# Kernel tuning notes

Hardware: AMD Instinct MI355X
Metric: run time of the kernel (lower is better)

## Reference

```python
import jax, jax.numpy as jnp
import numpy as np

B, S, H = 2, 2048, 2048
NH = 16
NOPE, ROPE, VDIM, RANK = 128, 64, 128, 512
QHD = NOPE + ROPE  # 192
MAX_POS, THETA = 4096, 50000.0
EPS = 1e-6


def rms_norm(x, w):
    var = jnp.mean(x.astype(jnp.float32) ** 2, axis=-1, keepdims=True)
    return (x * jax.lax.rsqrt(var + EPS)).astype(x.dtype) * w


def deinterleave(x):
    # view(..., d//2, 2).transpose(-1,-2).reshape(..., d): [x0,x2,...,x1,x3,...]
    return jnp.concatenate([x[..., ::2], x[..., 1::2]], axis=-1)


def rotate_half(x):
    x1, x2 = jnp.split(x, 2, axis=-1)
    return jnp.concatenate([-x2, x1], axis=-1)


def setup_inputs() -> dict:
    key = jax.random.key(0)
    ks = jax.random.split(key, 6)
    hidden_states = jax.random.normal(ks[0], (B, S, H), dtype=jnp.float32)
    attention_mask = jnp.broadcast_to(jnp.tril(jnp.ones((S, S), dtype=bool))[None, None], (B, 1, S, S))
    position_ids = jnp.broadcast_to(jnp.arange(S, dtype=jnp.int32)[None], (B, S))
    inv_freq = 1.0 / (THETA ** (jnp.arange(0, ROPE, 2, dtype=jnp.float32) / ROPE))
    freqs = jnp.arange(MAX_POS, dtype=jnp.float32)[:, None] * inv_freq[None, :]
    emb = jnp.concatenate([freqs, freqs], axis=-1)
    cos_cache, sin_cache = jnp.cos(emb), jnp.sin(emb)
    Wq = jax.random.normal(ks[1], (H, NH * QHD), dtype=jnp.float32) * 0.02
    Wkv_a = jax.random.normal(ks[2], (H, RANK + ROPE), dtype=jnp.float32) * 0.02
    kv_a_ln_w = jnp.ones((RANK,), dtype=jnp.float32)
    Wkv_b = jax.random.normal(ks[3], (NH, NOPE + VDIM, RANK), dtype=jnp.float32) * 0.02
    Wo = jax.random.normal(ks[4], (NH * VDIM, H), dtype=jnp.float32) * 0.02
    return {"hidden_states": hidden_states, "attention_mask": attention_mask, "position_ids": position_ids,
            "cos_cache": cos_cache, "sin_cache": sin_cache, "Wq": Wq, "Wkv_a": Wkv_a,
            "kv_a_ln_w": kv_a_ln_w, "Wkv_b": Wkv_b, "Wo": Wo}


def reference(hidden_states, attention_mask, position_ids, cos_cache, sin_cache, Wq, Wkv_a, kv_a_ln_w, Wkv_b, Wo):
    bsz, q_len, _ = hidden_states.shape
    scale = QHD ** (-0.5)
    # Q projection: [b,s,h*192] -> [b,h,s,192]
    q = (hidden_states @ Wq).reshape(bsz, q_len, NH, QHD).transpose(0, 2, 1, 3)
    q_nope, q_pe = q[..., :NOPE], q[..., NOPE:]
    # compressed KV + shared rope key: [b,s,576]
    ckv_full = hidden_states @ Wkv_a
    compressed_kv, k_pe = ckv_full[..., :RANK], ckv_full[..., RANK:]
    compressed_kv = rms_norm(compressed_kv, kv_a_ln_w)  # [b,s,512]
    # interleaved -> half layout, then standard RoPE
    q_pe = deinterleave(q_pe)                     # [b,h,s,64]
    k_pe = deinterleave(k_pe)                     # [b,s,64]
    cos = cos_cache[position_ids][:, None]        # [b,1,s,64]
    sin = sin_cache[position_ids][:, None]
    q_pe = q_pe * cos + rotate_half(q_pe) * sin
    k_pe = (k_pe[:, None] * cos + rotate_half(k_pe[:, None]) * sin)[:, 0]  # [b,s,64]
    # weight absorption
    q_absorb = Wkv_b[:, :NOPE]    # [h,128,512]
    out_absorb = Wkv_b[:, NOPE:]  # [h,128,512]
    q_nope_c = jnp.einsum('hdc,bhqd->bhqc', q_absorb, q_nope)  # [b,h,s,512]
    scores = (jnp.einsum('bhqd,bkd->bhqk', q_pe, k_pe)
              + jnp.einsum('bhqc,bkc->bhqk', q_nope_c, compressed_kv)) * scale
    scores = jnp.where(attention_mask, scores, jnp.float32(-1e9))
    probs = jax.nn.softmax(scores.astype(jnp.float32), axis=-1).astype(hidden_states.dtype)
    x = jnp.einsum('bhqk,bkc->bhqc', probs, compressed_kv)     # [b,h,s,512]
    attn = jnp.einsum('bhqc,hdc->bhqd', x, out_absorb)         # [b,h,s,128]
    attn = attn.transpose(0, 2, 1, 3).reshape(bsz, q_len, NH * VDIM)
    return attn @ Wo
```

## Files before the change

kernel.cpp:

```cpp
#include <hip/hip_runtime.h>
#include <math.h>

#define B_    2
#define S_    2048
#define H_    2048
#define NH_   16
#define NOPE_ 128
#define ROPE_ 64
#define VDIM_ 128
#define RANK_ 512
#define QHD_  192
#define DTOT_ 576

typedef short short8 __attribute__((ext_vector_type(8)));
typedef float f32x4 __attribute__((ext_vector_type(4)));

__device__ __forceinline__ unsigned short f2bf(float f) {
    unsigned u = __float_as_uint(f);
    u += 0x7fffu + ((u >> 16) & 1u);
    return (unsigned short)(u >> 16);
}
__device__ __forceinline__ float bf2f(unsigned short u) {
    return __uint_as_float((unsigned)u << 16);
}
__device__ __forceinline__ unsigned pack2bf(float a, float b) {
    return (unsigned)f2bf(a) | ((unsigned)f2bf(b) << 16);
}
__device__ __forceinline__ unsigned long long pack4bf(float a, float b, float c, float d) {
    return (unsigned long long)pack2bf(a, b) | ((unsigned long long)pack2bf(c, d) << 32);
}
union i4s8 { int4 i; short8 s; };

typedef __attribute__((address_space(3))) unsigned int lds_u32_t;
typedef __attribute__((address_space(1))) const unsigned int glob_u32_t;
__device__ __forceinline__ void async_copy16(const unsigned short* g, unsigned short* l) {
    __builtin_amdgcn_global_load_lds((glob_u32_t*)g, (lds_u32_t*)l, 16, 0, 0);
}

__global__ __launch_bounds__(256) void cast_bf16(const float* __restrict__ in,
                                                 unsigned short* __restrict__ out)
{
    const size_t i = ((size_t)blockIdx.x * 256 + threadIdx.x) * 4;
    float4 v = *(const float4*)(in + i);
    *(unsigned long long*)(out + i) = pack4bf(v.x, v.y, v.z, v.w);
}

__global__ __launch_bounds__(256) void transpose_w(const float* __restrict__ in,
                                                   unsigned short* __restrict__ out,
                                                   int Rr, int Cc,
                                                   size_t inBatch, size_t outBatch)
{
    __shared__ unsigned short tl[64][72];
    in  += (size_t)blockIdx.z * inBatch;
    out += (size_t)blockIdx.z * outBatch;
    const int t  = threadIdx.x;
    const int r0 = blockIdx.x * 64;
    const int c0 = blockIdx.y * 64;
    const int lr = t >> 4;
    const int lc = (t & 15) * 4;
#pragma unroll
    for (int r = 0; r < 4; ++r) {
        float4 v = *(const float4*)(in + (size_t)(r0 + lr*4 + r) * Cc + c0 + lc);
        tl[lr*4 + r][lc+0] = f2bf(v.x); tl[lr*4 + r][lc+1] = f2bf(v.y);
        tl[lr*4 + r][lc+2] = f2bf(v.z); tl[lr*4 + r][lc+3] = f2bf(v.w);
    }
    __syncthreads();
#pragma unroll
    for (int r = 0; r < 4; ++r) {
        ushort4 v;
        v.x = tl[lc+0][lr*4+r]; v.y = tl[lc+1][lr*4+r];
        v.z = tl[lc+2][lr*4+r]; v.w = tl[lc+3][lr*4+r];
        *(ushort4*)(out + (size_t)(c0 + lr*4 + r) * Rr + r0 + lc) = v;
    }
}

#define BGEMM_BODY(STORE_STMT)                                                     \
    __shared__ unsigned short Al[128*32];                                          \
    __shared__ unsigned short Bl[128*32];                                          \
    const int t = threadIdx.x;                                                     \
    const int wv = t >> 6;                                                         \
    const int lane = t & 63;                                                       \
    const int lq = lane & 15, quad = lane >> 4;                                    \
    const int m0 = blockIdx.y * 128, n0 = blockIdx.x * 128;                        \
    const int wrow = (wv >> 1) * 64, wcol = (wv & 1) * 64;                         \
    const int srow = lane >> 2;                                                    \
    const int scol = (lane & 3) * 8;                                               \
    f32x4 acc[4][4] = {};                                                          \
    for (int k0 = 0; k0 < K; k0 += 32) {                                           \
        _Pragma("unroll")                                                          \
        for (int pA = 0; pA < 2; ++pA) {                                           \
            const unsigned short* src =                                            \
                A + (size_t)(m0 + pA*64 + wv*16 + srow) * lda + k0 + scol;         \
            async_copy16(src, &Al[pA*2048 + wv*512]);                              \
        }                                                                          \
        _Pragma("unroll")                                                          \
        for (int pB = 0; pB < 2; ++pB) {                                           \
            int brow = n0 + pB*64 + wv*16 + srow;                                  \
            if (brow > N - 1) brow = N - 1;                                        \
            const unsigned short* src = B + (size_t)brow * ldb + k0 + scol;        \
            async_copy16(src, &Bl[pB*2048 + wv*512]);                              \
        }                                                                          \
        __syncthreads();                                                           \
        short8 af[4], bf[4];                                                       \
        _Pragma("unroll")                                                          \
        for (int i = 0; i < 4; ++i) {                                              \
            af[i] = *(const short8*)&Al[(wrow + i*16 + lq)*32 + quad*8];           \
            bf[i] = *(const short8*)&Bl[(wcol + i*16 + lq)*32 + quad*8];           \
        }                                                                          \
        _Pragma("unroll")                                                          \
        for (int mi = 0; mi < 4; ++mi)                                             \
            _Pragma("unroll")                                                      \
            for (int ni = 0; ni < 4; ++ni)                                         \
                acc[mi][ni] = __builtin_amdgcn_mfma_f32_16x16x32_bf16(             \
                    af[mi], bf[ni], acc[mi][ni], 0, 0, 0);                         \
        __syncthreads();                                                           \
    }                                                                              \
    _Pragma("unroll")                                                              \
    for (int mi = 0; mi < 4; ++mi)                                                 \
        _Pragma("unroll")                                                          \
        for (int ni = 0; ni < 4; ++ni) {                                           \
            int col = n0 + wcol + ni*16 + lq;                                      \
            if (col < N) {                                                         \
                _Pragma("unroll")                                                  \
                for (int r = 0; r < 4; ++r)                                        \
                    STORE_STMT;                                                    \
            }                                                                      \
        }

__global__ __launch_bounds__(256, 2) void bgemm2(const unsigned short* __restrict__ A,
                                                 int lda,
                                                 const unsigned short* __restrict__ B,
                                                 int ldb,
                                                 unsigned short* __restrict__ C,
                                                 int ldc, int K, int N, int qcmode)
{
    if (qcmode == 1) {
        const int z = blockIdx.z;
        A += (size_t)(z >> 4) * S_ * (NH_*QHD_) + (z & 15) * QHD_;
        B += (size_t)(z & 15) * RANK_ * NOPE_;
        C += (size_t)z * S_ * DTOT_;
    } else if (qcmode == 2) {
        const int z = blockIdx.z;
        A += (size_t)(z & 15) * 256 * RANK_ + (size_t)NOPE_ * RANK_;
        B += (size_t)(z >> 4) * S_ * DTOT_;
        C += (size_t)z * VDIM_ * S_;
    }
    BGEMM_BODY(C[(size_t)(m0 + wrow + mi*16 + quad*4 + r) * ldc + col] = f2bf(acc[mi][ni][r]))
}

__global__ __launch_bounds__(256, 2) void bgemm2f(const unsigned short* __restrict__ A,
                                                  int lda,
                                                  const unsigned short* __restrict__ B,
                                                  int ldb,
                                                  float* __restrict__ C,
                                                  int ldc, int K, int N)
{
    BGEMM_BODY(C[(size_t)(m0 + wrow + mi*16 + quad*4 + r) * ldc + col] = acc[mi][ni][r])
}

__global__ __launch_bounds__(128) void postkv(const unsigned short* __restrict__ ckv_bf,
                                              const float* __restrict__ lnw,
                                              const int*   __restrict__ pos_ids,
                                              const float* __restrict__ cosc,
                                              const float* __restrict__ sinc,
                                              unsigned short* __restrict__ k_cat)
{
    const int row = blockIdx.x;
    const int t   = threadIdx.x;
    const unsigned short* src = ckv_bf + (size_t)row * DTOT_;
    __shared__ float red[128];

    ushort4 v = *(const ushort4*)(src + t * 4);
    float x0 = bf2f(v.x), x1 = bf2f(v.y), x2 = bf2f(v.z), x3 = bf2f(v.w);
    red[t] = x0*x0 + x1*x1 + x2*x2 + x3*x3;
    __syncthreads();
    for (int off = 64; off > 0; off >>= 1) {
        if (t < off) red[t] += red[t + off];
        __syncthreads();
    }
    const float rs = rsqrtf(red[0] / (float)RANK_ + 1e-6f);

    unsigned short* kc = k_cat + (size_t)row * DTOT_;
    *(unsigned long long*)(kc + t*4) =
        pack4bf(x0*rs*lnw[t*4+0], x1*rs*lnw[t*4+1], x2*rs*lnw[t*4+2], x3*rs*lnw[t*4+3]);

    if (t < 32) {
        const int pos = pos_ids[row];
        const float c  = cosc[pos * ROPE_ + t];
        const float sn = sinc[pos * ROPE_ + t];
        const float y0 = bf2f(src[RANK_ + 2*t]);
        const float y1 = bf2f(src[RANK_ + 2*t + 1]);
        kc[RANK_ + t]      = f2bf(y0*c - y1*sn);
        kc[RANK_ + 32 + t] = f2bf(y1*c + y0*sn);
    }
}

__global__ __launch_bounds__(512) void ropeq(const unsigned short* __restrict__ q_bf,
                                             const int*   __restrict__ pos_ids,
                                             const float* __restrict__ cosc,
                                             const float* __restrict__ sinc,
                                             unsigned short* __restrict__ q_cat)
{
    const int row = blockIdx.x;
    const int t   = threadIdx.x;
    const int h   = t >> 5;
    const int i   = t & 31;
    const int pos = pos_ids[row];
    const float c  = cosc[pos * ROPE_ + i];
    const float sn = sinc[pos * ROPE_ + i];
    const unsigned short* qrow = q_bf + (size_t)row * (NH_*QHD_) + h * QHD_ + NOPE_;
    const float x0 = bf2f(qrow[2*i]);
    const float x1 = bf2f(qrow[2*i + 1]);
    const int b = row >> 11, s = row & 2047;
    unsigned short* qc = q_cat + ((size_t)(b * NH_ + h) * S_ + s) * DTOT_ + RANK_;
    qc[i]      = f2bf(x0*c - x1*sn);
    qc[32 + i] = f2bf(x1*c + x0*sn);
}

__global__ __launch_bounds__(256) void wcast(const float* __restrict__ w,
                                             unsigned short* __restrict__ wbf)
{
    const size_t i = ((size_t)blockIdx.x * 256 + threadIdx.x) * 4;
    float4 v = *(const float4*)(w + i);
    *(unsigned long long*)(wbf + i) = pack4bf(v.x, v.y, v.z, v.w);
}

__device__ __forceinline__ short8 quad_transpose(unsigned d0, unsigned d1,
                                                 unsigned d2, unsigned d3,
                                                 int srcA, int srcB, bool lowquad)
{
    int e0 = __shfl((int)d0, srcA, 64);
    int e1 = __shfl((int)d1, srcA, 64);
    int e2 = __shfl((int)d2, srcA, 64);
    int e3 = __shfl((int)d3, srcA, 64);
    int f0 = __shfl((int)d0, srcB, 64);
    int f1 = __shfl((int)d1, srcB, 64);
    int f2 = __shfl((int)d2, srcB, 64);
    int f3 = __shfl((int)d3, srcB, 64);
    i4s8 u;
    u.i.x = lowquad ? e0 : e2;
    u.i.y = lowquad ? e1 : e3;
    u.i.z = lowquad ? f0 : f2;
    u.i.w = lowquad ? f1 : f3;
    return u.s;
}

__global__ __launch_bounds__(256, 2) void flash_attn4(
    const unsigned short* __restrict__ q_cat,
    const unsigned short* __restrict__ k_cat,
    const unsigned short* __restrict__ vwt,
    unsigned short* __restrict__ attn_bf)
{
    __shared__ unsigned short sKa[32*512];
    __shared__ unsigned short sKb[32*64];
    __shared__ unsigned short sVW[128*32];

    const int t    = threadIdx.x;
    const int wv   = t >> 6;
    const int lane = t & 63;
    const int lq   = lane & 15;
    const int quad = lane >> 4;
    const int h    = blockIdx.x;
    const int q0   = (31 - blockIdx.y) * 64;
    const int b    = blockIdx.z;
    const int srcA = lq + ((quad & 1) << 5);
    const int srcB = srcA + 16;
    const bool lowq = quad < 2;
    const int myq  = q0 + wv*16 + lq;

    const unsigned short* qrow =
        q_cat + (((size_t)(b*NH_ + h)) * S_ + q0 + wv*16 + lq) * DTOT_ + quad*8;
    short8 qf[18];
#pragma unroll
    for (int c = 0; c < 18; ++c) qf[c] = *(const short8*)(qrow + c*32);

    const unsigned short* kcb = k_cat + (size_t)b * S_ * DTOT_;
    const unsigned short* vtb = vwt + (size_t)(b*NH_ + h) * VDIM_ * S_;

    f32x4 o[8];
#pragma unroll
    for (int i = 0; i < 8; ++i) o[i] = (f32x4){0.f, 0.f, 0.f, 0.f};
    float m_i = -1e30f, l_i = 0.f;
    const float scale = 0.0721687836f;
    const int ntiles = (q0 >> 5) + 2;

    const int swz  = lq & 7;
    const int selA = (swz >> 2) * 32;
    const int selB = 32 - selA;
    const int kqo  = (quad ^ (swz & 3)) * 8;
    const unsigned short* kr0a = &sKa[lq*512 + kqo];
    const unsigned short* kr1a = &sKa[(16 + lq)*512 + kqo];
    const unsigned short* kr0b = &sKb[lq*64 + kqo];
    const unsigned short* kr1b = &sKb[(16 + lq)*64 + kqo];

    const int kq0 = wv*DTOT_ + (lane ^ wv)*8;
    const int kq1 = wv*DTOT_ + (lane ^ (wv + 4))*8;
    const int kob = (t >> 3)*DTOT_ + RANK_ + ((t & 7) ^ ((t >> 3) & 7))*8;

    const int vrow  = wv*16 + (lane >> 2);
    const int vgcol = (((lane & 3) ^ ((lane >> 3) & 3))) * 8;
    const int pvsw  = (quad ^ ((lq >> 1) & 3)) * 8;

#define ISSUE_K(TPTR)                                                          \
    _Pragma("unroll")                                                          \
    for (int p = 0; p < 8; ++p)                                                \
        async_copy16((TPTR) + (p*4)*DTOT_ + ((p & 1) ? kq1 : kq0),             \
                     &sKa[p*2048 + wv*512]);                                   \
    async_copy16((TPTR) + kob, &sKb[wv*512])

    const unsigned short* ktp = kcb;
    ISSUE_K(ktp);
    ktp += 32 * DTOT_;

    for (int tt = 0; tt < ntiles; ++tt) {
        const int k0 = tt << 5;
        __syncthreads();
        {
#pragma unroll
            for (int p = 0; p < 2; ++p) {
                const unsigned short* vsrc =
                    vtb + (size_t)(p*64 + vrow) * S_ + k0 + vgcol;
                async_copy16(vsrc, &sVW[p*2048 + wv*512]);
            }
        }
        f32x4 s0a = {0.f,0.f,0.f,0.f}, s0b = {0.f,0.f,0.f,0.f};
        f32x4 s1a = {0.f,0.f,0.f,0.f}, s1b = {0.f,0.f,0.f,0.f};
#pragma unroll
        for (int c = 0; c < 16; c += 2) {
            short8 ka0 = *(const short8*)(kr0a + c*32 + selA);
            short8 kb0 = *(const short8*)(kr0a + c*32 + selB);
            short8 ka1 = *(const short8*)(kr1a + c*32 + selA);
            short8 kb1 = *(const short8*)(kr1a + c*32 + selB);
            s0a = __builtin_amdgcn_mfma_f32_16x16x32_bf16(ka0, qf[c],   s0a, 0, 0, 0);
            s1a = __builtin_amdgcn_mfma_f32_16x16x32_bf16(ka1, qf[c],   s1a, 0, 0, 0);
            s0b = __builtin_amdgcn_mfma_f32_16x16x32_bf16(kb0, qf[c+1], s0b, 0, 0, 0);
            s1b = __builtin_amdgcn_mfma_f32_16x16x32_bf16(kb1, qf[c+1], s1b, 0, 0, 0);
        }
        {
            short8 ka0 = *(const short8*)(kr0b + selA);
            short8 kb0 = *(const short8*)(kr0b + selB);
            short8 ka1 = *(const short8*)(kr1b + selA);
            short8 kb1 = *(const short8*)(kr1b + selB);
            s0a = __builtin_amdgcn_mfma_f32_16x16x32_bf16(ka0, qf[16], s0a, 0, 0, 0);
            s1a = __builtin_amdgcn_mfma_f32_16x16x32_bf16(ka1, qf[16], s1a, 0, 0, 0);
            s0b = __builtin_amdgcn_mfma_f32_16x16x32_bf16(kb0, qf[17], s0b, 0, 0, 0);
            s1b = __builtin_amdgcn_mfma_f32_16x16x32_bf16(kb1, qf[17], s1b, 0, 0, 0);
        }
        float sv[8];
#pragma unroll
        for (int r = 0; r < 4; ++r) {
            int kk0 = k0 + quad*4 + r;
            sv[r]     = (kk0      <= myq) ? (s0a[r] + s0b[r]) * scale : -1e30f;
            sv[r + 4] = (kk0 + 16 <= myq) ? (s1a[r] + s1b[r]) * scale : -1e30f;
        }
        float mx = sv[0];
#pragma unroll
        for (int i = 1; i < 8; ++i) mx = fmaxf(mx, sv[i]);
        mx = fmaxf(mx, __shfl_xor(mx, 16));
        mx = fmaxf(mx, __shfl_xor(mx, 32));
        if (!__all(mx <= m_i + 8.f)) {
            const float m_new = fmaxf(m_i, mx);
            const float alpha = __expf(m_i - m_new);
            m_i = m_new;
            l_i *= alpha;
#pragma unroll
            for (int i = 0; i < 8; ++i) {
                o[i][0]*=alpha; o[i][1]*=alpha; o[i][2]*=alpha; o[i][3]*=alpha;
            }
        }
        float p[8]; float ls = 0.f;
#pragma unroll
        for (int i = 0; i < 8; ++i) { p[i] = __expf(sv[i] - m_i); ls += p[i]; }
        ls += __shfl_xor(ls, 16);
        ls += __shfl_xor(ls, 32);
        l_i += ls;
        short8 pb = quad_transpose(pack2bf(p[0], p[1]), pack2bf(p[2], p[3]),
                                   pack2bf(p[4], p[5]), pack2bf(p[6], p[7]),
                                   srcA, srcB, lowq);
        __syncthreads();
        if (tt + 1 < ntiles) {
            ISSUE_K(ktp);
            ktp += 32 * DTOT_;
        }
#pragma unroll
        for (int dt = 0; dt < 8; ++dt) {
            short8 va = *(const short8*)&sVW[(dt*16 + lq)*32 + pvsw];
            o[dt] = __builtin_amdgcn_mfma_f32_16x16x32_bf16(va, pb, o[dt], 0, 0, 0);
        }
    }

    const float inv = 1.0f / l_i;
    unsigned short* orow =
        attn_bf + ((size_t)b * S_ + q0 + wv*16 + lq) * (NH_*VDIM_) + h*VDIM_;
#pragma unroll
    for (int dt2 = 0; dt2 < 4; ++dt2) {
        short8 xa = quad_transpose(
            pack2bf(o[2*dt2][0]*inv,   o[2*dt2][1]*inv),
            pack2bf(o[2*dt2][2]*inv,   o[2*dt2][3]*inv),
            pack2bf(o[2*dt2+1][0]*inv, o[2*dt2+1][1]*inv),
            pack2bf(o[2*dt2+1][2]*inv, o[2*dt2+1][3]*inv),
            srcA, srcB, lowq);
        *(short8*)(orow + dt2*32 + quad*8) = xa;
    }
}

extern "C" void kernel_launch(void* const* d_in, const int* in_sizes, int n_in,
                              void* d_out, int out_size, void* d_ws, size_t ws_size,
                              hipStream_t stream)
{
    const float* hidden  = (const float*)d_in[0];
    const int*   pos_ids = (const int*)d_in[2];
    const float* cosc    = (const float*)d_in[3];
    const float* sinc    = (const float*)d_in[4];
    const float* Wq      = (const float*)d_in[5];
    const float* Wkv_a   = (const float*)d_in[6];
    const float* lnw     = (const float*)d_in[7];
    const float* Wkv_b   = (const float*)d_in[8];
    const float* Wo      = (const float*)d_in[9];
    float* out = (float*)d_out;

    const int M = B_ * S_;
    char* ws = (char*)d_ws;
    unsigned short* hidden_bf = (unsigned short*)ws;
    unsigned short* vwT       = (unsigned short*)ws;
    unsigned short* q_bf      = (unsigned short*)(ws + 16777216);
    unsigned short* attn_bf   = q_bf;
    unsigned short* ckv_bf    = (unsigned short*)(ws + 41943040);
    unsigned short* wqaT      = ckv_bf;
    unsigned short* q_cat     = (unsigned short*)(ws + 46661632);
    unsigned short* k_cat     = (unsigned short*)(ws + 122159104);
    unsigned short* wT        = (unsigned short*)(ws + 126877696);
    unsigned short* w2bf      = (unsigned short*)(ws + 126877696 + 8388608);

    cast_bf16<<<8192, 256, 0, stream>>>(hidden, hidden_bf);
    transpose_w<<<dim3(32, 48, 1), 256, 0, stream>>>(Wq, wT, H_, NH_*QHD_, 0, 0);
    bgemm2<<<dim3(24, 32, 1), 256, 0, stream>>>(hidden_bf, H_, wT, H_, q_bf, NH_*QHD_, H_, NH_*QHD_, 0);
    transpose_w<<<dim3(32, 9, 1), 256, 0, stream>>>(Wkv_a, wT, H_, DTOT_, 0, 0);
    bgemm2<<<dim3(5, 32, 1), 256, 0, stream>>>(hidden_bf, H_, wT, H_, ckv_bf, DTOT_, H_, DTOT_, 0);
    postkv<<<M, 128, 0, stream>>>(ckv_bf, lnw, pos_ids, cosc, sinc, k_cat);
    ropeq<<<M, 512, 0, stream>>>(q_bf, pos_ids, cosc, sinc, q_cat);
    wcast<<<(NH_*256*RANK_)/1024, 256, 0, stream>>>(Wkv_b, w2bf);
    bgemm2<<<dim3(16, 1, 32), 256, 0, stream>>>(w2bf, RANK_, k_cat, DTOT_, vwT, S_, RANK_, S_, 2);
    transpose_w<<<dim3(2, 8, 16), 256, 0, stream>>>(Wkv_b, wqaT, NOPE_, RANK_,
                                                    (size_t)256*RANK_, (size_t)RANK_*NOPE_);
    bgemm2<<<dim3(4, 16, 32), 256, 0, stream>>>(q_bf, NH_*QHD_, wqaT, NOPE_, q_cat, DTOT_, NOPE_, RANK_, 1);
    flash_attn4<<<dim3(NH_, S_/64, B_), 256, 0, stream>>>(q_cat, k_cat, vwT, attn_bf);
    transpose_w<<<dim3(32, 32, 1), 256, 0, stream>>>(Wo, wT, H_, H_, 0, 0);
    bgemm2f<<<dim3(16, 32, 1), 256, 0, stream>>>(attn_bf, H_, wT, H_, out, H_, H_, H_);
}
```

Before: 523.6 us.

## Process two 64-row query strips per attention block to reuse K/V tiles

The flash attention kernel now handles 128 query rows per block: each wave keeps a second 16-row query group whose Q fragments are read from global memory inside the loop, along with a second set of online-softmax state and output accumulators. Each K/V tile staged in LDS is reused by twice as many queries, which halves the grid and the total K/V load traffic. The strip order is also reversed for one batch so heavy and light causal strips interleave across the grid. The costs are much higher register pressure from the doubled accumulators, repeated global loads of the second Q group on every tile, fewer blocks to balance the causal work, and a few extra masked tiles at the diagonal.

Result: slower. 621.2 us (+18.7%).

```diff
diff --git a/kernel.cpp b/kernel.cpp
--- a/kernel.cpp
+++ b/kernel.cpp
@@ -122,7 +122,7 @@
             int col = n0 + wcol + ni*16 + lq;                                      \
             if (col < N) {                                                         \
                 _Pragma("unroll")                                                  \
-                for (int r = 0; r < 4; ++r)                                        \
+                for (int r = 0; r < 4; ++r)                                       \
                     STORE_STMT;                                                    \
             }                                                                      \
         }
@@ -261,28 +261,33 @@
     const int lq   = lane & 15;
     const int quad = lane >> 4;
     const int h    = blockIdx.x;
-    const int q0   = (31 - blockIdx.y) * 64;
     const int b    = blockIdx.z;
+    const int ystrip = b ? blockIdx.y : (15 - blockIdx.y);
+    const int q0   = ystrip * 128;
     const int srcA = lq + ((quad & 1) << 5);
     const int srcB = srcA + 16;
     const bool lowq = quad < 2;
-    const int myq  = q0 + wv*16 + lq;
+    const int myq0 = q0 + wv*16 + lq;
 
     const unsigned short* qrow =
         q_cat + (((size_t)(b*NH_ + h)) * S_ + q0 + wv*16 + lq) * DTOT_ + quad*8;
     short8 qf[18];
 #pragma unroll
     for (int c = 0; c < 18; ++c) qf[c] = *(const short8*)(qrow + c*32);
+    const unsigned short* q1row = qrow + (size_t)64 * DTOT_;
 
     const unsigned short* kcb = k_cat + (size_t)b * S_ * DTOT_;
     const unsigned short* vtb = vwt + (size_t)(b*NH_ + h) * VDIM_ * S_;
 
-    f32x4 o[8];
-#pragma unroll
-    for (int i = 0; i < 8; ++i) o[i] = (f32x4){0.f, 0.f, 0.f, 0.f};
-    float m_i = -1e30f, l_i = 0.f;
+    f32x4 o0[8], o1[8];
+#pragma unroll
+    for (int i = 0; i < 8; ++i) {
+        o0[i] = (f32x4){0.f, 0.f, 0.f, 0.f};
+        o1[i] = (f32x4){0.f, 0.f, 0.f, 0.f};
+    }
+    float mi0 = -1e30f, li0 = 0.f, mi1 = -1e30f, li1 = 0.f;
     const float scale = 0.0721687836f;
-    const int ntiles = (q0 >> 5) + 2;
+    const int ntiles = (q0 >> 5) + 4;
 
     const int swz  = lq & 7;
     const int selA = (swz >> 2) * 32;
@@ -325,58 +330,89 @@
         }
         f32x4 s0a = {0.f,0.f,0.f,0.f}, s0b = {0.f,0.f,0.f,0.f};
         f32x4 s1a = {0.f,0.f,0.f,0.f}, s1b = {0.f,0.f,0.f,0.f};
+        f32x4 u0a = {0.f,0.f,0.f,0.f}, u0b = {0.f,0.f,0.f,0.f};
+        f32x4 u1a = {0.f,0.f,0.f,0.f}, u1b = {0.f,0.f,0.f,0.f};
 #pragma unroll
         for (int c = 0; c < 16; c += 2) {
             short8 ka0 = *(const short8*)(kr0a + c*32 + selA);
             short8 kb0 = *(const short8*)(kr0a + c*32 + selB);
             short8 ka1 = *(const short8*)(kr1a + c*32 + selA);
             short8 kb1 = *(const short8*)(kr1a + c*32 + selB);
+            short8 g1a = *(const short8*)(q1row + c*32);
+            short8 g1b = *(const short8*)(q1row + (c+1)*32);
             s0a = __builtin_amdgcn_mfma_f32_16x16x32_bf16(ka0, qf[c],   s0a, 0, 0, 0);
             s1a = __builtin_amdgcn_mfma_f32_16x16x32_bf16(ka1, qf[c],   s1a, 0, 0, 0);
             s0b = __builtin_amdgcn_mfma_f32_16x16x32_bf16(kb0, qf[c+1], s0b, 0, 0, 0);
             s1b = __builtin_amdgcn_mfma_f32_16x16x32_bf16(kb1, qf[c+1], s1b, 0, 0, 0);
+            u0a = __builtin_amdgcn_mfma_f32_16x16x32_bf16(ka0, g1a,     u0a, 0, 0, 0);
+            u1a = __builtin_amdgcn_mfma_f32_16x16x32_bf16(ka1, g1a,     u1a, 0, 0, 0);
+            u0b = __builtin_amdgcn_mfma_f32_16x16x32_bf16(kb0, g1b,     u0b, 0, 0, 0);
+            u1b = __builtin_amdgcn_mfma_f32_16x16x32_bf16(kb1, g1b,     u1b, 0, 0, 0);
         }
         {
             short8 ka0 = *(const short8*)(kr0b + selA);
             short8 kb0 = *(const short8*)(kr0b + selB);
             short8 ka1 = *(const short8*)(kr1b + selA);
             short8 kb1 = *(const short8*)(kr1b + selB);
+            short8 g1a = *(const short8*)(q1row + 16*32);
+            short8 g1b = *(const short8*)(q1row + 17*32);
             s0a = __builtin_amdgcn_mfma_f32_16x16x32_bf16(ka0, qf[16], s0a, 0, 0, 0);
             s1a = __builtin_amdgcn_mfma_f32_16x16x32_bf16(ka1, qf[16], s1a, 0, 0, 0);
             s0b = __builtin_amdgcn_mfma_f32_16x16x32_bf16(kb0, qf[17], s0b, 0, 0, 0);
             s1b = __builtin_amdgcn_mfma_f32_16x16x32_bf16(kb1, qf[17], s1b, 0, 0, 0);
-        }
-        float sv[8];
+            u0a = __builtin_amdgcn_mfma_f32_16x16x32_bf16(ka0, g1a,    u0a, 0, 0, 0);
+            u1a = __builtin_amdgcn_mfma_f32_16x16x32_bf16(ka1, g1a,    u1a, 0, 0, 0);
+            u0b = __builtin_amdgcn_mfma_f32_16x16x32_bf16(kb0, g1b,    u0b, 0, 0, 0);
+            u1b = __builtin_amdgcn_mfma_f32_16x16x32_bf16(kb1, g1b,    u1b, 0, 0, 0);
+        }
+        float sv0[8], sv1[8];
 #pragma unroll
         for (int r = 0; r < 4; ++r) {
             int kk0 = k0 + quad*4 + r;
-            sv[r]     = (kk0      <= myq) ? (s0a[r] + s0b[r]) * scale : -1e30f;
-            sv[r + 4] = (kk0 + 16 <= myq) ? (s1a[r] + s1b[r]) * scale : -1e30f;
-        }
-        float mx = sv[0];
-#pragma unroll
-        for (int i = 1; i < 8; ++i) mx = fmaxf(mx, sv[i]);
-        mx = fmaxf(mx, __shfl_xor(mx, 16));
-        mx = fmaxf(mx, __shfl_xor(mx, 32));
-        if (!__all(mx <= m_i + 8.f)) {
-            const float m_new = fmaxf(m_i, mx);
-            const float alpha = __expf(m_i - m_new);
-            m_i = m_new;
-            l_i *= alpha;
+            sv0[r]     = (kk0      <= myq0)      ? (s0a[r] + s0b[r]) * scale : -1e30f;
+            sv0[r + 4] = (kk0 + 16 <= myq0)      ? (s1a[r] + s1b[r]) * scale : -1e30f;
+            sv1[r]     = (kk0      <= myq0 + 64) ? (u0a[r] + u0b[r]) * scale : -1e30f;
+            sv1[r + 4] = (kk0 + 16 <= myq0 + 64) ? (u1a[r] + u1b[r]) * scale : -1e30f;
+        }
+        float mx0 = sv0[0], mx1 = sv1[0];
+#pragma unroll
+        for (int i = 1; i < 8; ++i) { mx0 = fmaxf(mx0, sv0[i]); mx1 = fmaxf(mx1, sv1[i]); }
+        mx0 = fmaxf(mx0, __shfl_xor(mx0, 16));
+        mx0 = fmaxf(mx0, __shfl_xor(mx0, 32));
+        mx1 = fmaxf(mx1, __shfl_xor(mx1, 16));
+        mx1 = fmaxf(mx1, __shfl_xor(mx1, 32));
+        if (!__all(mx0 <= mi0 + 8.f)) {
+            const float m_new = fmaxf(mi0, mx0);
+            const float alpha = __expf(mi0 - m_new);
+            mi0 = m_new; li0 *= alpha;
 #pragma unroll
             for (int i = 0; i < 8; ++i) {
-                o[i][0]*=alpha; o[i][1]*=alpha; o[i][2]*=alpha; o[i][3]*=alpha;
+                o0[i][0]*=alpha; o0[i][1]*=alpha; o0[i][2]*=alpha; o0[i][3]*=alpha;
             }
         }
-        float p[8]; float ls = 0.f;
-#pragma unroll
-        for (int i = 0; i < 8; ++i) { p[i] = __expf(sv[i] - m_i); ls += p[i]; }
-        ls += __shfl_xor(ls, 16);
-        ls += __shfl_xor(ls, 32);
-        l_i += ls;
-        short8 pb = quad_transpose(pack2bf(p[0], p[1]), pack2bf(p[2], p[3]),
-                                   pack2bf(p[4], p[5]), pack2bf(p[6], p[7]),
-                                   srcA, srcB, lowq);
+        if (!__all(mx1 <= mi1 + 8.f)) {
+            const float m_new = fmaxf(mi1, mx1);
+            const float alpha = __expf(mi1 - m_new);
+            mi1 = m_new; li1 *= alpha;
+#pragma unroll
+            for (int i = 0; i < 8; ++i) {
+                o1[i][0]*=alpha; o1[i][1]*=alpha; o1[i][2]*=alpha; o1[i][3]*=alpha;
+            }
+        }
+        float p0[8], p1[8]; float ls0 = 0.f, ls1 = 0.f;
+#pragma unroll
+        for (int i = 0; i < 8; ++i) {
+            p0[i] = __expf(sv0[i] - mi0); ls0 += p0[i];
+            p1[i] = __expf(sv1[i] - mi1); ls1 += p1[i];
+        }
+        ls0 += __shfl_xor(ls0, 16); ls0 += __shfl_xor(ls0, 32); li0 += ls0;
+        ls1 += __shfl_xor(ls1, 16); ls1 += __shfl_xor(ls1, 32); li1 += ls1;
+        short8 pb0 = quad_transpose(pack2bf(p0[0], p0[1]), pack2bf(p0[2], p0[3]),
+                                    pack2bf(p0[4], p0[5]), pack2bf(p0[6], p0[7]),
+                                    srcA, srcB, lowq);
+        short8 pb1 = quad_transpose(pack2bf(p1[0], p1[1]), pack2bf(p1[2], p1[3]),
+                                    pack2bf(p1[4], p1[5]), pack2bf(p1[6], p1[7]),
+                                    srcA, srcB, lowq);
         __syncthreads();
         if (tt + 1 < ntiles) {
             ISSUE_K(ktp);
@@ -385,22 +421,32 @@
 #pragma unroll
         for (int dt = 0; dt < 8; ++dt) {
             short8 va = *(const short8*)&sVW[(dt*16 + lq)*32 + pvsw];
-            o[dt] = __builtin_amdgcn_mfma_f32_16x16x32_bf16(va, pb, o[dt], 0, 0, 0);
-        }
-    }
-
-    const float inv = 1.0f / l_i;
+            o0[dt] = __builtin_amdgcn_mfma_f32_16x16x32_bf16(va, pb0, o0[dt], 0, 0, 0);
+            o1[dt] = __builtin_amdgcn_mfma_f32_16x16x32_bf16(va, pb1, o1[dt], 0, 0, 0);
+        }
+    }
+
+    const float inv0 = 1.0f / li0;
+    const float inv1 = 1.0f / li1;
     unsigned short* orow =
         attn_bf + ((size_t)b * S_ + q0 + wv*16 + lq) * (NH_*VDIM_) + h*VDIM_;
+    unsigned short* orow1 = orow + (size_t)64 * (NH_*VDIM_);
 #pragma unroll
     for (int dt2 = 0; dt2 < 4; ++dt2) {
         short8 xa = quad_transpose(
-            pack2bf(o[2*dt2][0]*inv,   o[2*dt2][1]*inv),
-            pack2bf(o[2*dt2][2]*inv,   o[2*dt2][3]*inv),
-            pack2bf(o[2*dt2+1][0]*inv, o[2*dt2+1][1]*inv),
-            pack2bf(o[2*dt2+1][2]*inv, o[2*dt2+1][3]*inv),
+            pack2bf(o0[2*dt2][0]*inv0,   o0[2*dt2][1]*inv0),
+            pack2bf(o0[2*dt2][2]*inv0,   o0[2*dt2][3]*inv0),
+            pack2bf(o0[2*dt2+1][0]*inv0, o0[2*dt2+1][1]*inv0),
+            pack2bf(o0[2*dt2+1][2]*inv0, o0[2*dt2+1][3]*inv0),
             srcA, srcB, lowq);
         *(short8*)(orow + dt2*32 + quad*8) = xa;
+        short8 xb = quad_transpose(
+            pack2bf(o1[2*dt2][0]*inv1,   o1[2*dt2][1]*inv1),
+            pack2bf(o1[2*dt2][2]*inv1,   o1[2*dt2][3]*inv1),
+            pack2bf(o1[2*dt2+1][0]*inv1, o1[2*dt2+1][1]*inv1),
+            pack2bf(o1[2*dt2+1][2]*inv1, o1[2*dt2+1][3]*inv1),
+            srcA, srcB, lowq);
+        *(short8*)(orow1 + dt2*32 + quad*8) = xb;
     }
 }
 
@@ -444,7 +490,7 @@
     transpose_w<<<dim3(2, 8, 16), 256, 0, stream>>>(Wkv_b, wqaT, NOPE_, RANK_,
                                                     (size_t)256*RANK_, (size_t)RANK_*NOPE_);
     bgemm2<<<dim3(4, 16, 32), 256, 0, stream>>>(q_bf, NH_*QHD_, wqaT, NOPE_, q_cat, DTOT_, NOPE_, RANK_, 1);
-    flash_attn4<<<dim3(NH_, S_/64, B_), 256, 0, stream>>>(q_cat, k_cat, vwT, attn_bf);
+    flash_attn4<<<dim3(NH_, S_/128, B_), 256, 0, stream>>>(q_cat, k_cat, vwT, attn_bf);
     transpose_w<<<dim3(32, 32, 1), 256, 0, stream>>>(Wo, wT, H_, H_, 0, 0);
     bgemm2f<<<dim3(16, 32, 1), 256, 0, stream>>>(attn_bf, H_, wT, H_, out, H_, H_, H_);
 }
```
